# Performance work log

Measured on AMD Instinct MI355X. Metric: run time of the kernel, lower is better.

## Reference

```python
import jax, jax.numpy as jnp
import numpy as np

ATOM_DIMS = [119, 5, 12, 12, 10, 6, 6, 2, 2]  # OGB full_atom_feature_dims
OFFSETS = np.concatenate([[0], np.cumsum(ATOM_DIMS[:-1])]).astype(np.int64)
N, E, H, NH = 100000, 1600000, 64, 8
DH = H // NH  # head_dim = 8


def setup_inputs() -> dict:
    key = jax.random.key(0)
    ks = jax.random.split(key, 24)
    # atom features, in-range per column
    X = jnp.stack([jax.random.randint(ks[i], (N,), 0, d) for i, d in enumerate(ATOM_DIMS)], axis=1)
    row = jax.random.randint(ks[9], (E,), 0, N)
    col = jax.random.randint(ks[10], (E,), 0, N)
    s = 1.0 / np.sqrt(H)
    atom_emb = jax.random.normal(ks[11], (int(sum(ATOM_DIMS)), H), jnp.float32)
    Wq = jax.random.normal(ks[12], (H, H), jnp.float32) * s
    bq = jnp.zeros((H,), jnp.float32)
    Wk = jax.random.normal(ks[13], (H, H), jnp.float32) * s
    bk = jnp.zeros((H,), jnp.float32)
    Wv = jax.random.normal(ks[14], (H, H), jnp.float32) * s
    bv = jnp.zeros((H,), jnp.float32)
    Wo = jax.random.normal(ks[15], (H, H), jnp.float32) * s
    bo = jnp.zeros((H,), jnp.float32)
    return {"X": X, "row": row, "col": col, "atom_emb": atom_emb,
            "Wq": Wq, "bq": bq, "Wk": Wk, "bk": bk, "Wv": Wv, "bv": bv,
            "Wo": Wo, "bo": bo}


def reference(X, row, col, atom_emb, Wq, bq, Wk, bk, Wv, bv, Wo, bo):
    offs = jnp.asarray(OFFSETS)
    # AtomEncoder: sum of per-feature embeddings -> [N, H]
    h = atom_emb[X + offs[None, :]].sum(axis=1)
    scaling = DH ** -0.5
    # linear projections, reshape to (N, head_dim, n_heads) as in SparseMHA
    q = (h @ Wq + bq).reshape(N, DH, NH) * scaling
    k = (h @ Wk + bk).reshape(N, DH, NH)
    v = (h @ Wv + bv).reshape(N, DH, NH)
    # SDDMM on sparse pattern: score[e, h] = sum_d q[row_e, d, h] * k[col_e, d, h]
    score = jnp.einsum('edh,edh->eh', q[row], k[col])  # [E, NH]
    # row-wise sparse softmax (per destination row of A, per head)
    m = jax.ops.segment_max(score, row, num_segments=N)  # [N, NH]
    p = jnp.exp(score - m[row])
    ssum = jax.ops.segment_sum(p, row, num_segments=N)  # [N, NH]
    attn = p / ssum[row]  # [E, NH]
    # SpMM: out[i, d, h] = sum_{e: row_e = i} attn[e, h] * v[col_e, d, h]
    out = jax.ops.segment_sum(attn[:, None, :] * v[col], row, num_segments=N)  # [N, DH, NH]
    return out.reshape(N, H) @ Wo + bo
```

## Files before the change

### kernel.cpp

```cpp
#include <hip/hip_runtime.h>
#include <hip/hip_bf16.h>
#include <hip/hip_fp16.h>


#define NPB 4
#define CAP 64
#define PSHIFT 8
#define PROWS 256
#define PCAP 4608
#define P1B 512

struct h4pack { __half2 a, b; };

__global__ void prep_weights_kernel(const float* __restrict__ Wq, const float* __restrict__ bq,
                                    const float* __restrict__ Wk, const float* __restrict__ bk,
                                    const float* __restrict__ Wv, const float* __restrict__ bv,
                                    float* __restrict__ wT, float* __restrict__ bT)
{
    const int t = threadIdx.x;
    for (int idx = t; idx < 64 * 192; idx += 256) {
        const int kk = idx / 192;
        const int c = idx % 192;
        const int sec = c >> 6;
        const int tcol = c & 63;
        const int oc = ((tcol & 7) << 3) | (tcol >> 3);
        float val;
        if (sec == 0)      val = Wq[kk * 64 + oc];
        else if (sec == 1) val = Wk[kk * 64 + oc];
        else               val = Wv[kk * 64 + oc];
        wT[idx] = val;
    }
    if (t < 192) {
        const int sec = t >> 6;
        const int tcol = t & 63;
        const int oc = ((tcol & 7) << 3) | (tcol >> 3);
        bT[t] = (sec == 0) ? bq[oc] : (sec == 1) ? bk[oc] : bv[oc];
    }
}

__global__ void __launch_bounds__(256)
encode_gemm_kernel(const int* __restrict__ X,
                   const float* __restrict__ atom_emb,
                   const float* __restrict__ wT, const float* __restrict__ bT,
                   float* __restrict__ qT, __half* __restrict__ kvh, int N)
{
    __shared__ float sH[64][68];

    const int tid = threadIdx.x;
    const int wv = tid >> 6, lane = tid & 63;
    const int nbase = blockIdx.x * 64;
    const int offs[9] = {0, 119, 124, 136, 148, 158, 164, 170, 172};
    for (int nn = 0; nn < 16; ++nn) {
        const int nloc = wv * 16 + nn;
        const int n = nbase + nloc;
        float hval = 0.f;
        if (n < N) {
#pragma unroll
            for (int f = 0; f < 9; ++f)
                hval += atom_emb[(size_t)(X[n * 9 + f] + offs[f]) * 64 + lane];
        }
        sH[nloc][lane] = hval;
    }
    __syncthreads();

    const int ng = tid >> 4;
    const int cg = tid & 15;

    float acc[4][12];
    {
        const float4 b0 = *(const float4*)&bT[4 * cg];
        const float4 b1 = *(const float4*)&bT[64 + 4 * cg];
        const float4 b2 = *(const float4*)&bT[128 + 4 * cg];
#pragma unroll
        for (int i = 0; i < 4; ++i) {
            acc[i][0] = b0.x; acc[i][1] = b0.y; acc[i][2]  = b0.z; acc[i][3]  = b0.w;
            acc[i][4] = b1.x; acc[i][5] = b1.y; acc[i][6]  = b1.z; acc[i][7]  = b1.w;
            acc[i][8] = b2.x; acc[i][9] = b2.y; acc[i][10] = b2.z; acc[i][11] = b2.w;
        }
    }

#define KSTEP(U, H0, H1, H2, H3)                                                    \
    {                                                                               \
        const float4 wq = *(const float4*)&wT[(kk + U) * 192 + 4 * cg];             \
        const float4 wk = *(const float4*)&wT[(kk + U) * 192 + 64 + 4 * cg];        \
        const float4 wv4 = *(const float4*)&wT[(kk + U) * 192 + 128 + 4 * cg];      \
        const float hh[4] = {H0, H1, H2, H3};                                       \
        _Pragma("unroll")                                                           \
        for (int i = 0; i < 4; ++i) {                                               \
            acc[i][0] = fmaf(hh[i], wq.x, acc[i][0]);                               \
            acc[i][1] = fmaf(hh[i], wq.y, acc[i][1]);                               \
            acc[i][2] = fmaf(hh[i], wq.z, acc[i][2]);                               \
            acc[i][3] = fmaf(hh[i], wq.w, acc[i][3]);                               \
            acc[i][4] = fmaf(hh[i], wk.x, acc[i][4]);                               \
            acc[i][5] = fmaf(hh[i], wk.y, acc[i][5]);                               \
            acc[i][6] = fmaf(hh[i], wk.z, acc[i][6]);                               \
            acc[i][7] = fmaf(hh[i], wk.w, acc[i][7]);                               \
            acc[i][8] = fmaf(hh[i], wv4.x, acc[i][8]);                              \
            acc[i][9] = fmaf(hh[i], wv4.y, acc[i][9]);                              \
            acc[i][10] = fmaf(hh[i], wv4.z, acc[i][10]);                            \
            acc[i][11] = fmaf(hh[i], wv4.w, acc[i][11]);                            \
        }                                                                           \
    }

    for (int kk = 0; kk < 64; kk += 4) {
        const float4 h0 = *(const float4*)&sH[ng * 4 + 0][kk];
        const float4 h1 = *(const float4*)&sH[ng * 4 + 1][kk];
        const float4 h2 = *(const float4*)&sH[ng * 4 + 2][kk];
        const float4 h3 = *(const float4*)&sH[ng * 4 + 3][kk];
        KSTEP(0, h0.x, h1.x, h2.x, h3.x)
        KSTEP(1, h0.y, h1.y, h2.y, h3.y)
        KSTEP(2, h0.z, h1.z, h2.z, h3.z)
        KSTEP(3, h0.w, h1.w, h2.w, h3.w)
    }
#undef KSTEP

#pragma unroll
    for (int i = 0; i < 4; ++i) {
        const int n = nbase + ng * 4 + i;
        if (n < N) {
            *(float4*)&qT[(size_t)n * 64 + 4 * cg] =
                make_float4(acc[i][0], acc[i][1], acc[i][2], acc[i][3]);
            h4pack kp, vp;
            kp.a = __floats2half2_rn(acc[i][4], acc[i][5]);
            kp.b = __floats2half2_rn(acc[i][6], acc[i][7]);
            vp.a = __floats2half2_rn(acc[i][8], acc[i][9]);
            vp.b = __floats2half2_rn(acc[i][10], acc[i][11]);
            *(h4pack*)&kvh[(size_t)n * 128 + 4 * cg] = kp;
            *(h4pack*)&kvh[(size_t)n * 128 + 64 + 4 * cg] = vp;
        }
    }
}

__global__ void __launch_bounds__(256)
partition_kernel(const int* __restrict__ row, const int* __restrict__ col,
                 int* __restrict__ pcursor, int2* __restrict__ pbuf,
                 int E, int NPART, int EPB)
{
    __shared__ int hist[512];
    __shared__ int base[512];

    const int tid = threadIdx.x;
    const int e0 = blockIdx.x * EPB;
    const int e1 = min(e0 + EPB, E);

    for (int i = tid; i < NPART; i += 256) hist[i] = 0;
    __syncthreads();

    for (int e = e0 + tid; e < e1; e += 256)
        atomicAdd(&hist[row[e] >> PSHIFT], 1);
    __syncthreads();

    for (int i = tid; i < NPART; i += 256) {
        const int h = hist[i];
        base[i] = h > 0 ? atomicAdd(&pcursor[i], h) : 0;
        hist[i] = 0;
    }
    __syncthreads();

    for (int e = e0 + tid; e < e1; e += 256) {
        const int r = row[e];
        const int p = r >> PSHIFT;
        const int pos = base[p] + atomicAdd(&hist[p], 1);
        if (pos < PCAP) pbuf[(size_t)p * PCAP + pos] = make_int2(r, col[e]);
    }
}

__global__ void __launch_bounds__(256)
bucket_kernel(const int* __restrict__ pcursor, const int2* __restrict__ pbuf,
              int* __restrict__ cnt, int* __restrict__ bucket, int N)
{
    __shared__ int lcnt[PROWS];

    const int p = blockIdx.x;
    const int tid = threadIdx.x;

    for (int i = tid; i < PROWS; i += 256) lcnt[i] = 0;
    __syncthreads();

    int nE = pcursor[p];
    if (nE > PCAP) nE = PCAP;
    const int2* buf = pbuf + (size_t)p * PCAP;

    for (int i = tid; i < nE; i += 256) {
        const int2 rc = buf[i];
        const int lr = rc.x & (PROWS - 1);
        const int pos = atomicAdd(&lcnt[lr], 1);
        if (pos < CAP) bucket[(size_t)rc.x * CAP + pos] = rc.y;
    }
    __syncthreads();

    const int rbase = p << PSHIFT;
    for (int i = tid; i < PROWS; i += 256) {
        const int r = rbase + i;
        if (r < N) cnt[r] = lcnt[i] < CAP ? lcnt[i] : CAP;
    }
}

__global__ void node_attn_kernel(const float* __restrict__ qT, const __half* __restrict__ kvh,
                                 const int* __restrict__ cnt, const int* __restrict__ bucket,
                                 const float* __restrict__ Wo, const float* __restrict__ bo,
                                 float* __restrict__ out, int N)
{
    __shared__ float sh[NPB][64];

    const int tid = threadIdx.x;
    const int g = tid >> 6;
    const int lane = tid & 63;
    const int eslot = lane >> 3;
    const int h = lane & 7;
    const int n = blockIdx.x * NPB + g;

    if (n < N) {
        const int d0 = cnt[n];
        const int d = d0 < CAP ? d0 : CAP;
        const int* bkt = bucket + (size_t)n * CAP;

        const float scaling = 0.35355339059327373f;
        float4 qa = *(const float4*)&qT[(size_t)n * 64 + h * 8];
        float4 qb = *(const float4*)&qT[(size_t)n * 64 + h * 8 + 4];
        qa.x *= scaling; qa.y *= scaling; qa.z *= scaling; qa.w *= scaling;
        qb.x *= scaling; qb.y *= scaling; qb.z *= scaling; qb.w *= scaling;

        float m = -3.4e38f, sumP = 0.f;
        float a0 = 0.f, a1 = 0.f, a2 = 0.f, a3 = 0.f;
        float a4 = 0.f, a5 = 0.f, a6 = 0.f, a7 = 0.f;

        for (int j0 = 0; j0 < d; j0 += 8) {
            const int myj = j0 + eslot;
            const bool valid = myj < d;
            const int c = bkt[valid ? myj : j0];
            const __half* kvb = kvh + (size_t)c * 128 + h * 8;
            const float4 kraw = *(const float4*)(kvb);
            const float4 vraw = *(const float4*)(kvb + 64);
            const __half2* kh = (const __half2*)&kraw;
            const __half2* vh = (const __half2*)&vraw;
            const float2 k0 = __half22float2(kh[0]);
            const float2 k1 = __half22float2(kh[1]);
            const float2 k2 = __half22float2(kh[2]);
            const float2 k3 = __half22float2(kh[3]);
            const float2 v0 = __half22float2(vh[0]);
            const float2 v1 = __half22float2(vh[1]);
            const float2 v2 = __half22float2(vh[2]);
            const float2 v3 = __half22float2(vh[3]);

            float s = qa.x * k0.x + qa.y * k0.y + qa.z * k1.x + qa.w * k1.y
                    + qb.x * k2.x + qb.y * k2.y + qb.z * k3.x + qb.w * k3.y;
            s = valid ? s : -3.4e38f;

            const float mNew = fmaxf(m, s);
            const float corr = __expf(m - mNew);
            const float p = valid ? __expf(s - mNew) : 0.f;
            sumP = fmaf(sumP, corr, p);
            a0 = fmaf(a0, corr, p * v0.x);
            a1 = fmaf(a1, corr, p * v0.y);
            a2 = fmaf(a2, corr, p * v1.x);
            a3 = fmaf(a3, corr, p * v1.y);
            a4 = fmaf(a4, corr, p * v2.x);
            a5 = fmaf(a5, corr, p * v2.y);
            a6 = fmaf(a6, corr, p * v3.x);
            a7 = fmaf(a7, corr, p * v3.y);
            m = mNew;
        }

#pragma unroll
        for (int mask = 8; mask <= 32; mask <<= 1) {
            const float mo = __shfl_xor(m, mask, 64);
            const float mN = fmaxf(m, mo);
            const float cs = __expf(m - mN);
            const float co = __expf(mo - mN);
            const float so = __shfl_xor(sumP, mask, 64);
            sumP = sumP * cs + so * co;
            float t;
            t = __shfl_xor(a0, mask, 64); a0 = a0 * cs + t * co;
            t = __shfl_xor(a1, mask, 64); a1 = a1 * cs + t * co;
            t = __shfl_xor(a2, mask, 64); a2 = a2 * cs + t * co;
            t = __shfl_xor(a3, mask, 64); a3 = a3 * cs + t * co;
            t = __shfl_xor(a4, mask, 64); a4 = a4 * cs + t * co;
            t = __shfl_xor(a5, mask, 64); a5 = a5 * cs + t * co;
            t = __shfl_xor(a6, mask, 64); a6 = a6 * cs + t * co;
            t = __shfl_xor(a7, mask, 64); a7 = a7 * cs + t * co;
            m = mN;
        }

        if (eslot == 0) {
            const float inv = (d > 0) ? 1.f / sumP : 0.f;
            sh[g][0 * 8 + h] = a0 * inv;
            sh[g][1 * 8 + h] = a1 * inv;
            sh[g][2 * 8 + h] = a2 * inv;
            sh[g][3 * 8 + h] = a3 * inv;
            sh[g][4 * 8 + h] = a4 * inv;
            sh[g][5 * 8 + h] = a5 * inv;
            sh[g][6 * 8 + h] = a6 * inv;
            sh[g][7 * 8 + h] = a7 * inv;
        }
    }
    __syncthreads();

    if (n < N) {
        float o = bo[lane];
#pragma unroll
        for (int i = 0; i < 64; ++i)
            o = fmaf(sh[g][i], Wo[i * 64 + lane], o);
        out[(size_t)n * 64 + lane] = o;
    }
}

extern "C" void kernel_launch(void* const* d_in, const int* in_sizes, int n_in,
                              void* d_out, int out_size, void* d_ws, size_t ws_size,
                              hipStream_t stream)
{
    const int*   X        = (const int*)d_in[0];
    const int*   row      = (const int*)d_in[1];
    const int*   col      = (const int*)d_in[2];
    const float* atom_emb = (const float*)d_in[3];
    const float* Wq       = (const float*)d_in[4];
    const float* bq       = (const float*)d_in[5];
    const float* Wk       = (const float*)d_in[6];
    const float* bk       = (const float*)d_in[7];
    const float* Wv       = (const float*)d_in[8];
    const float* bv       = (const float*)d_in[9];
    const float* Wo       = (const float*)d_in[10];
    const float* bo       = (const float*)d_in[11];

    const int N = in_sizes[0] / 9;
    const int E = in_sizes[1];
    const int NPART = (N + PROWS - 1) >> PSHIFT;
    const int EPB = (E + P1B - 1) / P1B;

    float*  qT   = (float*)d_ws;
    __half* kvh  = (__half*)(qT + (size_t)N * 64);
    int* cnt     = (int*)(kvh + (size_t)N * 128);
    int* bucket  = cnt + N;
    int* pcursor = bucket + (size_t)N * CAP;
    int2* pbuf   = (int2*)(pcursor + 512);
    float* wT    = (float*)(pbuf + (size_t)NPART * PCAP);
    float* bT    = wT + 64 * 192;

    hipMemsetAsync(pcursor, 0, 512 * sizeof(int), stream);

    prep_weights_kernel<<<1, 256, 0, stream>>>(Wq, bq, Wk, bk, Wv, bv, wT, bT);

    encode_gemm_kernel<<<(N + 63) / 64, 256, 0, stream>>>(
        X, atom_emb, wT, bT, qT, kvh, N);

    partition_kernel<<<P1B, 256, 0, stream>>>(row, col, pcursor, pbuf, E, NPART, EPB);

    bucket_kernel<<<NPART, 256, 0, stream>>>(pcursor, pbuf, cnt, bucket, N);

    node_attn_kernel<<<(N + NPB - 1) / NPB, 256, 0, stream>>>(
        qT, kvh, cnt, bucket, Wo, bo, (float*)d_out, N);
}
```

Baseline: 302.9 us.

## Merge partition into encode launch and use two-pass softmax in attention

The edge partition kernel is folded into the encode/GEMM kernel as extra leading blocks, so the two independent stages run in one launch and can overlap. The node attention loop moves from online softmax with per-edge rescaling to two passes. The first pass gathers K, computes scores and takes a wave-wide max. The second pass gathers V and accumulates without correction factors, and the cross-lane reduction becomes plain sums. This cuts exp and FMA work but holds up to 8 scores and column indices per lane in registers, so the loop is bounded to CAP=64 neighbours by unrolling.

Result: no change. 301.1 us (-0.6%).

```diff
diff --git a/kernel.cpp b/kernel.cpp
--- a/kernel.cpp
+++ b/kernel.cpp
@@ -39,16 +39,50 @@
 }
 
 __global__ void __launch_bounds__(256)
-encode_gemm_kernel(const int* __restrict__ X,
-                   const float* __restrict__ atom_emb,
-                   const float* __restrict__ wT, const float* __restrict__ bT,
-                   float* __restrict__ qT, __half* __restrict__ kvh, int N)
+encode_partition_kernel(const int* __restrict__ X,
+                        const float* __restrict__ atom_emb,
+                        const float* __restrict__ wT, const float* __restrict__ bT,
+                        const int* __restrict__ row, const int* __restrict__ col,
+                        int* __restrict__ pcursor, int2* __restrict__ pbuf,
+                        float* __restrict__ qT, __half* __restrict__ kvh,
+                        int N, int E, int NPART, int EPB)
 {
     __shared__ float sH[64][68];
 
     const int tid = threadIdx.x;
+
+    if (blockIdx.x < P1B) {
+        int* hist = (int*)sH;
+        int* base = hist + 512;
+
+        const int e0 = blockIdx.x * EPB;
+        const int e1 = min(e0 + EPB, E);
+
+        for (int i = tid; i < NPART; i += 256) hist[i] = 0;
+        __syncthreads();
+
+        for (int e = e0 + tid; e < e1; e += 256)
+            atomicAdd(&hist[row[e] >> PSHIFT], 1);
+        __syncthreads();
+
+        for (int i = tid; i < NPART; i += 256) {
+            const int hh = hist[i];
+            base[i] = hh > 0 ? atomicAdd(&pcursor[i], hh) : 0;
+            hist[i] = 0;
+        }
+        __syncthreads();
+
+        for (int e = e0 + tid; e < e1; e += 256) {
+            const int r = row[e];
+            const int p = r >> PSHIFT;
+            const int pos = base[p] + atomicAdd(&hist[p], 1);
+            if (pos < PCAP) pbuf[(size_t)p * PCAP + pos] = make_int2(r, col[e]);
+        }
+        return;
+    }
+
     const int wv = tid >> 6, lane = tid & 63;
-    const int nbase = blockIdx.x * 64;
+    const int nbase = (blockIdx.x - P1B) * 64;
     const int offs[9] = {0, 119, 124, 136, 148, 158, 164, 170, 172};
     for (int nn = 0; nn < 16; ++nn) {
         const int nloc = wv * 16 + nn;
@@ -132,40 +166,6 @@
 }
 
 __global__ void __launch_bounds__(256)
-partition_kernel(const int* __restrict__ row, const int* __restrict__ col,
-                 int* __restrict__ pcursor, int2* __restrict__ pbuf,
-                 int E, int NPART, int EPB)
-{
-    __shared__ int hist[512];
-    __shared__ int base[512];
-
-    const int tid = threadIdx.x;
-    const int e0 = blockIdx.x * EPB;
-    const int e1 = min(e0 + EPB, E);
-
-    for (int i = tid; i < NPART; i += 256) hist[i] = 0;
-    __syncthreads();
-
-    for (int e = e0 + tid; e < e1; e += 256)
-        atomicAdd(&hist[row[e] >> PSHIFT], 1);
-    __syncthreads();
-
-    for (int i = tid; i < NPART; i += 256) {
-        const int h = hist[i];
-        base[i] = h > 0 ? atomicAdd(&pcursor[i], h) : 0;
-        hist[i] = 0;
-    }
-    __syncthreads();
-
-    for (int e = e0 + tid; e < e1; e += 256) {
-        const int r = row[e];
-        const int p = r >> PSHIFT;
-        const int pos = base[p] + atomicAdd(&hist[p], 1);
-        if (pos < PCAP) pbuf[(size_t)p * PCAP + pos] = make_int2(r, col[e]);
-    }
-}
-
-__global__ void __launch_bounds__(256)
 bucket_kernel(const int* __restrict__ pcursor, const int2* __restrict__ pbuf,
               int* __restrict__ cnt, int* __restrict__ bucket, int N)
 {
@@ -221,65 +221,76 @@
         qa.x *= scaling; qa.y *= scaling; qa.z *= scaling; qa.w *= scaling;
         qb.x *= scaling; qb.y *= scaling; qb.z *= scaling; qb.w *= scaling;
 
-        float m = -3.4e38f, sumP = 0.f;
+        float s[8];
+        int   c[8];
+        float m = -3.4e38f;
+
+#pragma unroll
+        for (int it = 0; it < 8; ++it) {
+            if (it * 8 < d) {
+                const int myj = it * 8 + eslot;
+                const bool valid = myj < d;
+                const int cc = bkt[valid ? myj : it * 8];
+                c[it] = cc;
+                const __half* kp = kvh + (size_t)cc * 128 + h * 8;
+                const float4 kraw = *(const float4*)kp;
+                const __half2* kh = (const __half2*)&kraw;
+                const float2 k0 = __half22float2(kh[0]);
+                const float2 k1 = __half22float2(kh[1]);
+                const float2 k2 = __half22float2(kh[2]);
+                const float2 k3 = __half22float2(kh[3]);
+                float sc = qa.x * k0.x + qa.y * k0.y + qa.z * k1.x + qa.w * k1.y
+                         + qb.x * k2.x + qb.y * k2.y + qb.z * k3.x + qb.w * k3.y;
+                s[it] = valid ? sc : -3.4e38f;
+                m = fmaxf(m, s[it]);
+            } else {
+                s[it] = -3.4e38f;
+                c[it] = 0;
+            }
+        }
+
+        m = fmaxf(m, __shfl_xor(m, 8, 64));
+        m = fmaxf(m, __shfl_xor(m, 16, 64));
+        m = fmaxf(m, __shfl_xor(m, 32, 64));
+
+        float sumP = 0.f;
         float a0 = 0.f, a1 = 0.f, a2 = 0.f, a3 = 0.f;
         float a4 = 0.f, a5 = 0.f, a6 = 0.f, a7 = 0.f;
 
-        for (int j0 = 0; j0 < d; j0 += 8) {
-            const int myj = j0 + eslot;
-            const bool valid = myj < d;
-            const int c = bkt[valid ? myj : j0];
-            const __half* kvb = kvh + (size_t)c * 128 + h * 8;
-            const float4 kraw = *(const float4*)(kvb);
-            const float4 vraw = *(const float4*)(kvb + 64);
-            const __half2* kh = (const __half2*)&kraw;
-            const __half2* vh = (const __half2*)&vraw;
-            const float2 k0 = __half22float2(kh[0]);
-            const float2 k1 = __half22float2(kh[1]);
-            const float2 k2 = __half22float2(kh[2]);
-            const float2 k3 = __half22float2(kh[3]);
-            const float2 v0 = __half22float2(vh[0]);
-            const float2 v1 = __half22float2(vh[1]);
-            const float2 v2 = __half22float2(vh[2]);
-            const float2 v3 = __half22float2(vh[3]);
-
-            float s = qa.x * k0.x + qa.y * k0.y + qa.z * k1.x + qa.w * k1.y
-                    + qb.x * k2.x + qb.y * k2.y + qb.z * k3.x + qb.w * k3.y;
-            s = valid ? s : -3.4e38f;
-
-            const float mNew = fmaxf(m, s);
-            const float corr = __expf(m - mNew);
-            const float p = valid ? __expf(s - mNew) : 0.f;
-            sumP = fmaf(sumP, corr, p);
-            a0 = fmaf(a0, corr, p * v0.x);
-            a1 = fmaf(a1, corr, p * v0.y);
-            a2 = fmaf(a2, corr, p * v1.x);
-            a3 = fmaf(a3, corr, p * v1.y);
-            a4 = fmaf(a4, corr, p * v2.x);
-            a5 = fmaf(a5, corr, p * v2.y);
-            a6 = fmaf(a6, corr, p * v3.x);
-            a7 = fmaf(a7, corr, p * v3.y);
-            m = mNew;
+#pragma unroll
+        for (int it = 0; it < 8; ++it) {
+            if (it * 8 < d) {
+                const float p = __expf(s[it] - m);
+                sumP += p;
+                const __half* vp = kvh + (size_t)c[it] * 128 + 64 + h * 8;
+                const float4 vraw = *(const float4*)vp;
+                const __half2* vh = (const __half2*)&vraw;
+                const float2 v0 = __half22float2(vh[0]);
+                const float2 v1 = __half22float2(vh[1]);
+                const float2 v2 = __half22float2(vh[2]);
+                const float2 v3 = __half22float2(vh[3]);
+                a0 = fmaf(p, v0.x, a0);
+                a1 = fmaf(p, v0.y, a1);
+                a2 = fmaf(p, v1.x, a2);
+                a3 = fmaf(p, v1.y, a3);
+                a4 = fmaf(p, v2.x, a4);
+                a5 = fmaf(p, v2.y, a5);
+                a6 = fmaf(p, v3.x, a6);
+                a7 = fmaf(p, v3.y, a7);
+            }
         }
 
 #pragma unroll
         for (int mask = 8; mask <= 32; mask <<= 1) {
-            const float mo = __shfl_xor(m, mask, 64);
-            const float mN = fmaxf(m, mo);
-            const float cs = __expf(m - mN);
-            const float co = __expf(mo - mN);
-            const float so = __shfl_xor(sumP, mask, 64);
-            sumP = sumP * cs + so * co;
-            float t;
-            t = __shfl_xor(a0, mask, 64); a0 = a0 * cs + t * co;
-            t = __shfl_xor(a1, mask, 64); a1 = a1 * cs + t * co;
-            t = __shfl_xor(a2, mask, 64); a2 = a2 * cs + t * co;
-            t = __shfl_xor(a3, mask, 64); a3 = a3 * cs + t * co;
-            t = __shfl_xor(a4, mask, 64); a4 = a4 * cs + t * co;
-            t = __shfl_xor(a5, mask, 64); a5 = a5 * cs + t * co;
-            t = __shfl_xor(a6, mask, 64); a6 = a6 * cs + t * co;
-            t = __shfl_xor(a7, mask, 64); a7 = a7 * cs + t * co;
-            m = mN;
+            sumP += __shfl_xor(sumP, mask, 64);
+            a0 += __shfl_xor(a0, mask, 64);
+            a1 += __shfl_xor(a1, mask, 64);
+            a2 += __shfl_xor(a2, mask, 64);
+            a3 += __shfl_xor(a3, mask, 64);
+            a4 += __shfl_xor(a4, mask, 64);
+            a5 += __shfl_xor(a5, mask, 64);
+            a6 += __shfl_xor(a6, mask, 64);
+            a7 += __shfl_xor(a7, mask, 64);
         }
 
         if (eslot == 0) {
@@ -340,10 +351,9 @@
 
     prep_weights_kernel<<<1, 256, 0, stream>>>(Wq, bq, Wk, bk, Wv, bv, wT, bT);
 
-    encode_gemm_kernel<<<(N + 63) / 64, 256, 0, stream>>>(
-        X, atom_emb, wT, bT, qT, kvh, N);
-
-    partition_kernel<<<P1B, 256, 0, stream>>>(row, col, pcursor, pbuf, E, NPART, EPB);
+    const int encB = (N + 63) / 64;
+    encode_partition_kernel<<<P1B + encB, 256, 0, stream>>>(
+        X, atom_emb, wT, bT, row, col, pcursor, pbuf, qT, kvh, N, E, NPART, EPB);
 
     bucket_kernel<<<NPART, 256, 0, stream>>>(pcursor, pbuf, cnt, bucket, N);
 
```
